# Kernel optimization log

Measured on AMD Instinct MI355X. Metric: run time of the kernel, lower is better.

Reference implementation:

```python
import jax, jax.numpy as jnp
import numpy as np

N_NODES = 100000
N_EDGES = 3200000
NUM_GRAPHS = 128
DIM = 2


def setup_inputs() -> dict:
    key = jax.random.key(0)
    k1, k2, k3 = jax.random.split(key, 3)
    node_pos = jax.random.normal(k1, (N_NODES, DIM), dtype=jnp.float32)
    raw_edge_index = jax.random.randint(k2, (2, N_EDGES), 0, N_NODES, dtype=jnp.int64)
    batch = jnp.sort(jax.random.randint(k3, (N_NODES,), 0, NUM_GRAPHS, dtype=jnp.int64))
    return {"node_pos": node_pos, "raw_edge_index": raw_edge_index, "batch": batch}


def reference(node_pos, raw_edge_index, batch):
    # gather edge endpoints: [E, DIM]
    start = node_pos[raw_edge_index[0]]
    end = node_pos[raw_edge_index[1]]
    # per-edge (||end - start|| - 1)^2 : [E]
    eu = jnp.linalg.norm(end - start, axis=1)
    edge_var = jnp.square(eu - 1.0)
    # graph id of each edge (via its source node): [E]
    index = batch[raw_edge_index[0]]
    # scatter-mean by graph
    sums = jax.ops.segment_sum(edge_var, index, num_segments=NUM_GRAPHS)
    counts = jax.ops.segment_sum(jnp.ones_like(edge_var), index, num_segments=NUM_GRAPHS)
    graph_var = sums / jnp.maximum(counts, 1.0)
    # self.reduce defaults to torch.mean over graphs -> scalar
    return jnp.mean(graph_var)
```

## Files before the change

kernel.cpp:

```cpp
#include <hip/hip_runtime.h>

#define NGRAPH 128
#define NBLK   1024
#define BS     256


__global__ __launch_bounds__(BS) void edgevar_pack(
    const float2* __restrict__ pos,
    const int*    __restrict__ batch,
    float4*       __restrict__ packed,
    int N) {
  const int i = blockIdx.x * BS + threadIdx.x;
  if (i < N) {
    float2 p = pos[i];
    packed[i] = make_float4(p.x, p.y, __int_as_float(batch[i]), 0.f);
  }
}

__global__ __launch_bounds__(BS) void edgevar_stage1(
    const float4* __restrict__ packed,
    const int*    __restrict__ ei,
    float*        __restrict__ part,
    int E) {
  __shared__ float s_acc[2 * NGRAPH];
  s_acc[threadIdx.x] = 0.f;
  __syncthreads();

  const int tid = blockIdx.x * BS + threadIdx.x;
  const int nth = NBLK * BS;
  const int E4  = E >> 2;
  const int4*   __restrict__ s4  = (const int4*)ei;
  const int4*   __restrict__ d4  = (const int4*)(ei + E);
  const float2* __restrict__ pp2 = (const float2*)packed;

  for (int i = tid; i < E4; i += nth) {
    int4 s = s4[i];
    int4 d = d4[i];
    int ss[4] = {s.x, s.y, s.z, s.w};
    int dd[4] = {d.x, d.y, d.z, d.w};
#pragma unroll
    for (int k = 0; k < 4; ++k) {
      float4 a = packed[ss[k]];
      float2 b = pp2[2 * dd[k]];
      float dx = b.x - a.x, dy = b.y - a.y;
      float eu = sqrtf(dx * dx + dy * dy);
      float v  = eu - 1.f;
      v *= v;
      int g = __float_as_int(a.z);
      atomicAdd(&s_acc[g], v);
      atomicAdd(&s_acc[NGRAPH + g], 1.f);
    }
  }
  for (int e = (E4 << 2) + tid; e < E; e += nth) {
    float4 a = packed[ei[e]];
    float2 b = pp2[2 * ei[e + E]];
    float dx = b.x - a.x, dy = b.y - a.y;
    float eu = sqrtf(dx * dx + dy * dy);
    float v  = eu - 1.f;
    v *= v;
    int g = __float_as_int(a.z);
    atomicAdd(&s_acc[g], v);
    atomicAdd(&s_acc[NGRAPH + g], 1.f);
  }

  __syncthreads();
  part[(size_t)blockIdx.x * (2 * NGRAPH) + threadIdx.x] = s_acc[threadIdx.x];
}

__global__ __launch_bounds__(1024) void edgevar_stage2(
    const float* __restrict__ part,
    float*       __restrict__ out) {
  const int t    = threadIdx.x;
  const int slot = t & 255;
  const int rc   = t >> 8;
  const int ROWS = NBLK / 4;

  float acc = 0.f;
  const float* p = part + (size_t)rc * ROWS * 256 + slot;
#pragma unroll 8
  for (int r = 0; r < ROWS; ++r) acc += p[(size_t)r * 256];

  __shared__ float s1[1024];
  s1[t] = acc;
  __syncthreads();

  __shared__ float s2[256];
  if (t < 256) s2[t] = s1[t] + s1[t + 256] + s1[t + 512] + s1[t + 768];
  __syncthreads();

  __shared__ float var[NGRAPH];
  if (t < NGRAPH) var[t] = s2[t] / fmaxf(s2[NGRAPH + t], 1.f);
  __syncthreads();

  if (t < 64) {
    float v = var[t] + var[t + 64];
    for (int off = 32; off; off >>= 1) v += __shfl_down(v, off);
    if (t == 0) out[0] = v * (1.0f / NGRAPH);
  }
}

extern "C" void kernel_launch(void* const* d_in, const int* in_sizes, int n_in,
                              void* d_out, int out_size, void* d_ws, size_t ws_size,
                              hipStream_t stream) {
  const float2* pos   = (const float2*)d_in[0];
  const int*    ei    = (const int*)d_in[1];
  const int*    batch = (const int*)d_in[2];
  float*        out   = (float*)d_out;
  const int N = in_sizes[0] / 2;
  const int E = in_sizes[1] / 2;

  float4* packed = (float4*)d_ws;
  float*  part   = (float*)((char*)d_ws + (size_t)N * sizeof(float4));

  hipLaunchKernelGGL(edgevar_pack, dim3((N + BS - 1) / BS), dim3(BS), 0, stream,
                     pos, batch, packed, N);
  hipLaunchKernelGGL(edgevar_stage1, dim3(NBLK), dim3(BS), 0, stream,
                     packed, ei, part, E);
  hipLaunchKernelGGL(edgevar_stage2, dim3(1), dim3(1024), 0, stream,
                     part, out);
}
```

Before: 120.5 us.

## Pack count and fixed-point sum into one 64-bit LDS atomic, privatized 4 ways

Each edge now does one 64-bit integer atomicAdd into shared memory instead of two float atomics. The count sits in the high bits and a fixed-point squared-deviation value in the low 42 bits. The per-graph accumulators are also split into 4 copies indexed by thread lane mod 4, which reduces LDS atomic contention on hot graph slots. Stage2 is adapted to reduce the packed 64-bit partials. The cost is fixed-point quantization (2^-18 resolution per edge) and a risk of overflow if a graph's summed values exceed the 42-bit field.

Measured after the change: 116.0 us. -3.7%, faster.

```diff
diff --git a/kernel.cpp b/kernel.cpp
--- a/kernel.cpp
+++ b/kernel.cpp
@@ -3,6 +3,9 @@
 #define NGRAPH 128
 #define NBLK   1024
 #define BS     256
+
+#define FIX_SCALE 262144.0f
+#define CNT_SHIFT 42
 
 
 __global__ __launch_bounds__(BS) void edgevar_pack(
@@ -20,12 +23,19 @@
 __global__ __launch_bounds__(BS) void edgevar_stage1(
     const float4* __restrict__ packed,
     const int*    __restrict__ ei,
-    float*        __restrict__ part,
+    unsigned long long* __restrict__ part,
     int E) {
-  __shared__ float s_acc[2 * NGRAPH];
-  s_acc[threadIdx.x] = 0.f;
+  __shared__ unsigned long long s_acc[4][NGRAPH];
+  {
+    unsigned long long* f = &s_acc[0][0];
+    if (threadIdx.x < 2 * NGRAPH) {
+      f[threadIdx.x] = 0ull;
+      f[threadIdx.x + 2 * NGRAPH] = 0ull;
+    }
+  }
   __syncthreads();
 
+  const int cp  = threadIdx.x & 3;
   const int tid = blockIdx.x * BS + threadIdx.x;
   const int nth = NBLK * BS;
   const int E4  = E >> 2;
@@ -43,53 +53,61 @@
       float4 a = packed[ss[k]];
       float2 b = pp2[2 * dd[k]];
       float dx = b.x - a.x, dy = b.y - a.y;
-      float eu = sqrtf(dx * dx + dy * dy);
-      float v  = eu - 1.f;
+      float v  = sqrtf(dx * dx + dy * dy) - 1.f;
       v *= v;
       int g = __float_as_int(a.z);
-      atomicAdd(&s_acc[g], v);
-      atomicAdd(&s_acc[NGRAPH + g], 1.f);
+      unsigned long long contrib =
+          (1ull << CNT_SHIFT) | (unsigned long long)(v * FIX_SCALE + 0.5f);
+      atomicAdd(&s_acc[cp][g], contrib);
     }
   }
   for (int e = (E4 << 2) + tid; e < E; e += nth) {
     float4 a = packed[ei[e]];
     float2 b = pp2[2 * ei[e + E]];
     float dx = b.x - a.x, dy = b.y - a.y;
-    float eu = sqrtf(dx * dx + dy * dy);
-    float v  = eu - 1.f;
+    float v  = sqrtf(dx * dx + dy * dy) - 1.f;
     v *= v;
     int g = __float_as_int(a.z);
-    atomicAdd(&s_acc[g], v);
-    atomicAdd(&s_acc[NGRAPH + g], 1.f);
+    unsigned long long contrib =
+        (1ull << CNT_SHIFT) | (unsigned long long)(v * FIX_SCALE + 0.5f);
+    atomicAdd(&s_acc[cp][g], contrib);
   }
 
   __syncthreads();
-  part[(size_t)blockIdx.x * (2 * NGRAPH) + threadIdx.x] = s_acc[threadIdx.x];
+  if (threadIdx.x < NGRAPH) {
+    unsigned long long t = s_acc[0][threadIdx.x] + s_acc[1][threadIdx.x]
+                         + s_acc[2][threadIdx.x] + s_acc[3][threadIdx.x];
+    part[(size_t)blockIdx.x * NGRAPH + threadIdx.x] = t;
+  }
 }
 
 __global__ __launch_bounds__(1024) void edgevar_stage2(
-    const float* __restrict__ part,
-    float*       __restrict__ out) {
+    const unsigned long long* __restrict__ part,
+    float* __restrict__ out) {
   const int t    = threadIdx.x;
-  const int slot = t & 255;
-  const int rc   = t >> 8;
-  const int ROWS = NBLK / 4;
+  const int slot = t & (NGRAPH - 1);
+  const int rc   = t >> 7;
+  const int ROWS = NBLK / 8;
 
-  float acc = 0.f;
-  const float* p = part + (size_t)rc * ROWS * 256 + slot;
+  unsigned long long acc = 0ull;
+  const unsigned long long* p = part + (size_t)rc * ROWS * NGRAPH + slot;
 #pragma unroll 8
-  for (int r = 0; r < ROWS; ++r) acc += p[(size_t)r * 256];
+  for (int r = 0; r < ROWS; ++r) acc += p[(size_t)r * NGRAPH];
 
-  __shared__ float s1[1024];
-  s1[t] = acc;
-  __syncthreads();
-
-  __shared__ float s2[256];
-  if (t < 256) s2[t] = s1[t] + s1[t + 256] + s1[t + 512] + s1[t + 768];
+  __shared__ unsigned long long s[1024];
+  s[t] = acc;
   __syncthreads();
 
   __shared__ float var[NGRAPH];
-  if (t < NGRAPH) var[t] = s2[t] / fmaxf(s2[NGRAPH + t], 1.f);
+  if (t < NGRAPH) {
+    unsigned long long tot = 0ull;
+#pragma unroll
+    for (int j = 0; j < 8; ++j) tot += s[t + NGRAPH * j];
+    unsigned int       cnt = (unsigned int)(tot >> CNT_SHIFT);
+    unsigned long long fx  = tot & ((1ull << CNT_SHIFT) - 1ull);
+    float sum = (float)fx * (1.0f / FIX_SCALE);
+    var[t] = sum / fmaxf((float)cnt, 1.f);
+  }
   __syncthreads();
 
   if (t < 64) {
@@ -109,8 +127,9 @@
   const int N = in_sizes[0] / 2;
   const int E = in_sizes[1] / 2;
 
-  float4* packed = (float4*)d_ws;
-  float*  part   = (float*)((char*)d_ws + (size_t)N * sizeof(float4));
+  float4*             packed = (float4*)d_ws;
+  unsigned long long* part   =
+      (unsigned long long*)((char*)d_ws + (size_t)N * sizeof(float4));
 
   hipLaunchKernelGGL(edgevar_pack, dim3((N + BS - 1) / BS), dim3(BS), 0, stream,
                      pos, batch, packed, N);
```
